# Kernel optimization log

Measured on AMD Instinct MI355X. Metric: run time of the kernel, lower is better.

Reference implementation:

```python
import jax, jax.numpy as jnp
import numpy as np

B, C, H, W_ = 16, 512, 32, 32
NH = 8
DK = C // NH  # 64


def setup_inputs() -> dict:
    key = jax.random.key(0)
    ks = jax.random.split(key, 7)
    s = 1.0 / np.sqrt(C).astype(np.float32)
    x = jax.random.normal(ks[0], (B, C, H, W_), jnp.float32)
    # 1x1 convs == per-pixel channel matmuls; weight shape (out_c, in_c)
    w_q = jax.random.normal(ks[1], (C, C), jnp.float32) * s
    w_k = jax.random.normal(ks[2], (C, C), jnp.float32) * s
    w_v = jax.random.normal(ks[3], (C, C), jnp.float32) * s
    w_o = jax.random.normal(ks[4], (C, C), jnp.float32) * s
    b_o = jnp.zeros((C,), jnp.float32)
    ps = DK ** -0.5
    rel_h = jax.random.normal(ks[5], (2 * H - 1, DK), jnp.float32) * ps
    rel_w = jax.random.normal(ks[6], (2 * W_ - 1, DK), jnp.float32) * ps
    return dict(x=x, w_q=w_q, w_k=w_k, w_v=w_v, w_o=w_o, b_o=b_o,
                rel_h=rel_h, rel_w=rel_w)


def _rel_pos_bias(q, rel_h, rel_w):
    # q: (B, NH, H*W, DK). Content-aware 2D relative position bias:
    # bias[x,y,i,j] = q[x,y]·rel_w[j-y+W-1] + q[x,y]·rel_h[i-x+H-1]
    q4 = q.reshape(B, NH, H, W_, DK)
    idx_w = jnp.arange(W_)[None, :] - jnp.arange(W_)[:, None] + (W_ - 1)  # (Wq,Wk)
    idx_h = jnp.arange(H)[None, :] - jnp.arange(H)[:, None] + (H - 1)     # (Hq,Hk)
    lw = jnp.einsum('bnxyd,rd->bnxyr', q4, rel_w)                # (B,NH,H,W,2W-1)
    aw = jnp.take_along_axis(lw, idx_w[None, None, None], axis=-1)  # (B,NH,H,Wq,Wk)
    lh = jnp.einsum('bnxyd,rd->bnxyr', q4, rel_h)                # (B,NH,H,W,2H-1)
    ah = jnp.take_along_axis(lh.swapaxes(2, 3), idx_h[None, None, None], axis=-1)
    ah = ah.swapaxes(2, 3)                                       # (B,NH,Hq,Wq,Hk)
    bias = ah[..., :, None] + aw[..., None, :]                   # (B,NH,H,W,Hk,Wk)
    return bias.reshape(B, NH, H * W_, H * W_)


def reference(x, w_q, w_k, w_v, w_o, b_o, rel_h, rel_w):
    def proj(w):
        y = jnp.einsum('oc,bchw->bohw', w, x)
        # rearrange 'b (dk h) hi wi -> b h (hi wi) dk' (d_k outer, head inner)
        return y.reshape(B, DK, NH, H * W_).transpose(0, 2, 3, 1)

    q = proj(w_q)  # (B,NH,N,DK), N = H*W
    k = proj(w_k)
    v = proj(w_v)

    energy = jnp.einsum('bnqd,bnkd->bnqk', q, k)
    bias = _rel_pos_bias(q, rel_h, rel_w)
    scores = jax.nn.softmax((energy + bias) / np.sqrt(DK).astype(np.float32), axis=-1)
    out = jnp.einsum('bnqk,bnkd->bnqd', scores, v)
    # rearrange 'b h (hi wi) d -> b (h d) hi wi' (head outer, d_k inner)
    out = out.transpose(0, 1, 3, 2).reshape(B, C, H, W_)
    out = jnp.einsum('oc,bchw->bohw', w_o, out) + b_o[None, :, None, None]
    return out
```

## Files before the change

kernel.cpp:

```cpp
#include <hip/hip_runtime.h>

typedef __attribute__((ext_vector_type(8))) short s8v;
typedef __attribute__((ext_vector_type(4))) float f4v;
typedef __attribute__((ext_vector_type(4))) unsigned short u4v;
typedef __attribute__((ext_vector_type(2))) unsigned int u2v;
typedef __attribute__((ext_vector_type(4))) float fl4;

#define MFMA __builtin_amdgcn_mfma_f32_16x16x32_bf16
#define LOG2E 1.44269504088896340736f
#define QSCALE (0.125f * LOG2E)

__device__ __forceinline__ unsigned short f2bf(float f) {
  return (unsigned short)((__float_as_uint(f) + 0x8000u) >> 16);
}
__device__ __forceinline__ unsigned int pack_bf(float a, float b) {
  return __builtin_amdgcn_perm(__float_as_uint(b) + 0x8000u,
                               __float_as_uint(a) + 0x8000u, 0x07060302u);
}
__device__ __forceinline__ float bf2f(unsigned short u) {
  return __uint_as_float(((unsigned int)u) << 16);
}

__device__ __forceinline__ void gload16(const void* g, void* l) {
  __builtin_amdgcn_global_load_lds(
      (const __attribute__((address_space(1))) unsigned int*)g,
      (__attribute__((address_space(3))) unsigned int*)l,
      16, 0, 0);
}

__device__ __forceinline__ void stage64(unsigned short* lds,
                                        const unsigned short* src,
                                        int src_ld, int tid) {
  const int w = tid >> 6, l = tid & 63;
#pragma unroll
  for (int c = 0; c < 2; ++c) {
    int idx = (c * 4 + w) * 64 + l;
    int row = idx >> 3, cl = idx & 7;
    gload16(src + row * src_ld + ((cl ^ (row & 7)) << 3),
            lds + (c * 4 + w) * 512);
  }
}
__device__ __forceinline__ void stage128(unsigned short* lds,
                                         const unsigned short* src,
                                         int src_ld, int tid) {
  const int w = tid >> 6, l = tid & 63;
#pragma unroll
  for (int c = 0; c < 4; ++c) {
    int id = c * 256 + w * 64 + l;
    int row = id >> 3, cl = id & 7;
    gload16(src + row * src_ld + ((cl ^ (row & 7)) << 3),
            lds + (c * 256 + w * 64) * 8);
  }
}
__device__ __forceinline__ s8v frag64(const unsigned short* lds, int row, int chunk) {
  return *(const s8v*)(lds + row * 64 + ((chunk ^ (row & 7)) << 3));
}

__global__ void cvt_all(const float* __restrict__ wq, const float* __restrict__ wk,
                        const float* __restrict__ wv, const float* __restrict__ wo,
                        const float* __restrict__ relh, const float* __restrict__ relw,
                        unsigned short* __restrict__ Wqkv, unsigned short* __restrict__ Wob,
                        unsigned short* __restrict__ Rel) {
  const int bid = blockIdx.x, tid = threadIdx.x;
  if (bid < 768) {
    int i = bid * 256 + tid;
    int orow = i >> 7, c4 = (i & 127) * 4;
    int p = orow >> 9, oc = orow & 511;
    int h = oc >> 6, d = oc & 63;
    const float* w = (p == 0) ? wq : (p == 1) ? wk : wv;
    fl4 v = *(const fl4*)(w + (d * 8 + h) * 512 + c4);
    u4v o;
    o[0] = f2bf(v[0]); o[1] = f2bf(v[1]); o[2] = f2bf(v[2]); o[3] = f2bf(v[3]);
    *(u4v*)(Wqkv + orow * 512 + c4) = o;
  } else if (bid < 1024) {
    int i = (bid - 768) * 256 + tid;
    fl4 v = ((const fl4*)wo)[i];
    u4v o;
    o[0] = f2bf(v[0]); o[1] = f2bf(v[1]); o[2] = f2bf(v[2]); o[3] = f2bf(v[3]);
    ((u4v*)Wob)[i] = o;
  } else {
    int i = (bid - 1024) * 256 + tid;
    int t = i >> 12, r = (i >> 6) & 63, d = i & 63;
    const float* s = t ? relw : relh;
    Rel[i] = (r < 63) ? f2bf(s[r * 64 + d]) : (unsigned short)0;
  }
}

__global__ void xpose(const float* __restrict__ x, unsigned short* __restrict__ Xt) {
  __shared__ float tls[32][33];
  const int c0 = blockIdx.x * 32, n0 = blockIdx.y * 32, b = blockIdx.z;
  const int tid = threadIdx.x;
  const int rr = tid >> 3, cc4 = (tid & 7) * 4;
  fl4 v = *(const fl4*)(x + (b * 512 + c0 + rr) * 1024 + n0 + cc4);
#pragma unroll
  for (int i = 0; i < 4; ++i) tls[rr][cc4 + i] = v[i];
  __syncthreads();
  u4v o;
#pragma unroll
  for (int i = 0; i < 4; ++i) o[i] = f2bf(tls[cc4 + i][rr]);
  *(u4v*)(Xt + (b * 1024 + n0 + rr) * 512 + c0 + cc4) = o;
}

__global__ __launch_bounds__(256, 2)
void qkv_gemm(const unsigned short* __restrict__ W,
              const unsigned short* __restrict__ Xt,
              unsigned short* __restrict__ qb,
              unsigned short* __restrict__ kb,
              unsigned short* __restrict__ vtb) {
  __shared__ __align__(16) unsigned short Al[8192];
  __shared__ __align__(16) unsigned short Bl[8192];
  const int tid = threadIdx.x, w = tid >> 6, l = tid & 63;
  const int l15 = l & 15, lg = l >> 4;
  const int wr = w >> 1, wc = w & 1;
  const int m0 = blockIdx.x * 128, n0 = blockIdx.y * 128, b = blockIdx.z;
  f4v acc[4][4] = {};
  const unsigned short* As = W + m0 * 512;
  const unsigned short* Bs = Xt + (b * 1024 + n0) * 512;
  for (int k0 = 0; k0 < 512; k0 += 64) {
    stage128(Al, As + k0, 512, tid);
    stage128(Bl, Bs + k0, 512, tid);
    __syncthreads();
#pragma unroll
    for (int kk = 0; kk < 2; ++kk) {
      s8v a[4], bb[4];
#pragma unroll
      for (int i = 0; i < 4; ++i) a[i] = frag64(Al + wr * 4096, i * 16 + l15, kk * 4 + lg);
#pragma unroll
      for (int j = 0; j < 4; ++j) bb[j] = frag64(Bl + wc * 4096, j * 16 + l15, kk * 4 + lg);
#pragma unroll
      for (int i = 0; i < 4; ++i)
#pragma unroll
        for (int j = 0; j < 4; ++j)
          acc[i][j] = MFMA(a[i], bb[j], acc[i][j], 0, 0, 0);
    }
    __syncthreads();
  }
  const int p = m0 >> 9;
  const float sc = (p == 0) ? QSCALE : 1.0f;
#pragma unroll
  for (int i = 0; i < 4; ++i) {
    int o = m0 + wr * 64 + i * 16 + lg * 4;
    int oc = o & 511, hh = oc >> 6, dd = oc & 63;
#pragma unroll
    for (int j = 0; j < 4; ++j) {
      int n = n0 + wc * 64 + j * 16 + l15;
      if (p < 2) {
        u2v pk;
        pk[0] = pack_bf(acc[i][j][0] * sc, acc[i][j][1] * sc);
        pk[1] = pack_bf(acc[i][j][2] * sc, acc[i][j][3] * sc);
        unsigned short* dst = (p == 0 ? qb : kb) + (((b * 8 + hh) * 1024 + n) * 64 + dd);
        *(u2v*)dst = pk;
      } else {
#pragma unroll
        for (int r = 0; r < 4; ++r)
          vtb[((b * 8 + hh) * 64 + dd + r) * 1024 + n] = f2bf(acc[i][j][r]);
      }
    }
  }
}

__global__ __launch_bounds__(256, 4)
void attn_kernel(const unsigned short* __restrict__ qbuf,
                 const unsigned short* __restrict__ kbuf,
                 const unsigned short* __restrict__ vtbuf,
                 const unsigned short* __restrict__ relb,
                 unsigned short* __restrict__ AO) {
  __shared__ __align__(16) unsigned short SH[17152];
  unsigned short* Kl  = SH;
  unsigned short* Vl  = SH + 4096;
  unsigned short* lhb = SH + 8192;
  unsigned short* PwB = SH + 12544;

  const int tid = threadIdx.x, w = tid >> 6, l = tid & 63;
  const int l15 = l & 15, lg = l >> 4;
  const int q0 = blockIdx.x * 64;
  const int bh = blockIdx.z * 8 + blockIdx.y;
  const unsigned short* qh = qbuf + bh * 65536;
  const unsigned short* kh = kbuf + bh * 65536;
  const unsigned short* vh = vtbuf + bh * 65536;
  const int qloc = w * 16 + l15;
  const int qrow = q0 + qloc;
  const int x = qrow >> 5, y = qrow & 31;

  s8v bq[2];
#pragma unroll
  for (int kk = 0; kk < 2; ++kk)
    bq[kk] = *(const s8v*)(qh + qrow * 64 + kk * 32 + lg * 8);

  unsigned short* lwt = SH;
#pragma unroll
  for (int t = 0; t < 2; ++t) {
    unsigned short* dst = t ? lwt : lhb;
#pragma unroll
    for (int ct = 0; ct < 4; ++ct) {
      f4v c = {0.f, 0.f, 0.f, 0.f};
#pragma unroll
      for (int kk = 0; kk < 2; ++kk) {
        s8v a = *(const s8v*)(relb + t * 4096 + (ct * 16 + l15) * 64 + kk * 32 + lg * 8);
        c = MFMA(a, bq[kk], c, 0, 0, 0);
      }
      u2v pk;
      pk[0] = pack_bf(c[0], c[1]);
      pk[1] = pack_bf(c[2], c[3]);
      *(u2v*)(dst + qloc * 68 + ct * 16 + lg * 4) = pk;
    }
  }
  float lwreg[2][4];
#pragma unroll
  for (int c1 = 0; c1 < 2; ++c1)
#pragma unroll
    for (int r = 0; r < 4; ++r)
      lwreg[c1][r] = bf2f(lwt[qloc * 68 + (c1 * 16 + lg * 4 + r) - y + 31]);
  __syncthreads();

  float lsum = 0.f;
  f4v ao[4] = {};
  unsigned short* pw = PwB + w * 1152;

  for (int n0 = 0; n0 < 1024; n0 += 64) {
    stage64(Kl, kh + n0 * 64, 64, tid);
    stage64(Vl, vh + n0, 1024, tid);
    __syncthreads();

    int ib = qloc * 68 + (n0 >> 5) - x + 31;
    float lh0 = bf2f(lhb[ib]);
    float lh1 = bf2f(lhb[ib + 1]);

#pragma unroll
    for (int ct = 0; ct < 4; ++ct) {
      float lh = (ct & 2) ? lh1 : lh0;
      f4v c;
#pragma unroll
      for (int r = 0; r < 4; ++r) c[r] = lh + lwreg[ct & 1][r];
#pragma unroll
      for (int kk = 0; kk < 2; ++kk)
        c = MFMA(frag64(Kl, ct * 16 + l15, kk * 4 + lg), bq[kk], c, 0, 0, 0);
      f4v e;
#pragma unroll
      for (int r = 0; r < 4; ++r) e[r] = __builtin_amdgcn_exp2f(c[r]);
      lsum += (e[0] + e[1]) + (e[2] + e[3]);
      u2v pk;
      pk[0] = pack_bf(e[0], e[1]);
      pk[1] = pack_bf(e[2], e[3]);
      *(u2v*)(pw + l15 * 72 + ct * 16 + lg * 4) = pk;
    }

    s8v ap[2];
#pragma unroll
    for (int kk = 0; kk < 2; ++kk)
      ap[kk] = *(const s8v*)(pw + l15 * 72 + kk * 32 + lg * 8);
#pragma unroll
    for (int dt = 0; dt < 4; ++dt)
#pragma unroll
      for (int kk = 0; kk < 2; ++kk)
        ao[dt] = MFMA(frag64(Vl, dt * 16 + l15, kk * 4 + lg), ap[kk], ao[dt], 0, 0, 0);
    __syncthreads();
  }

  lsum += __shfl_xor(lsum, 16);
  lsum += __shfl_xor(lsum, 32);

  float inv = 1.0f / lsum;
#pragma unroll
  for (int dt = 0; dt < 4; ++dt) {
    u2v pk;
    pk[0] = pack_bf(ao[dt][0] * inv, ao[dt][1] * inv);
    pk[1] = pack_bf(ao[dt][2] * inv, ao[dt][3] * inv);
    *(u2v*)(AO + (bh * 1024 + qrow) * 64 + dt * 16 + lg * 4) = pk;
  }
}

__global__ __launch_bounds__(256, 2)
void out_gemm(const unsigned short* __restrict__ Wo,
              const unsigned short* __restrict__ AO,
              const float* __restrict__ bo,
              float* __restrict__ out) {
  __shared__ __align__(16) unsigned short Al[8192];
  __shared__ __align__(16) unsigned short Bl[8192];
  const int tid = threadIdx.x, w = tid >> 6, l = tid & 63;
  const int l15 = l & 15, lg = l >> 4;
  const int wr = w >> 1, wc = w & 1;
  const int m0 = blockIdx.x * 128, n0 = blockIdx.y * 128, b = blockIdx.z;
  f4v acc[4][4] = {};
  for (int k0 = 0; k0 < 512; k0 += 64) {
    stage128(Al, Wo + m0 * 512 + k0, 512, tid);
    stage128(Bl, AO + ((b * 8 + (k0 >> 6)) * 1024 + n0) * 64, 64, tid);
    __syncthreads();
#pragma unroll
    for (int kk = 0; kk < 2; ++kk) {
      s8v a[4], bb[4];
#pragma unroll
      for (int i = 0; i < 4; ++i) a[i] = frag64(Al + wr * 4096, i * 16 + l15, kk * 4 + lg);
#pragma unroll
      for (int j = 0; j < 4; ++j) bb[j] = frag64(Bl + wc * 4096, j * 16 + l15, kk * 4 + lg);
#pragma unroll
      for (int i = 0; i < 4; ++i)
#pragma unroll
        for (int j = 0; j < 4; ++j)
          acc[i][j] = MFMA(a[i], bb[j], acc[i][j], 0, 0, 0);
    }
    __syncthreads();
  }
#pragma unroll
  for (int i = 0; i < 4; ++i) {
    int ob = m0 + wr * 64 + i * 16 + lg * 4;
    float b0 = bo[ob], b1 = bo[ob + 1], b2 = bo[ob + 2], b3 = bo[ob + 3];
#pragma unroll
    for (int j = 0; j < 4; ++j) {
      int n = n0 + wc * 64 + j * 16 + l15;
      float* op = out + (b * 512 + ob) * 1024 + n;
      op[0]    = acc[i][j][0] + b0;
      op[1024] = acc[i][j][1] + b1;
      op[2048] = acc[i][j][2] + b2;
      op[3072] = acc[i][j][3] + b3;
    }
  }
}


extern "C" void kernel_launch(void* const* d_in, const int* in_sizes, int n_in,
                              void* d_out, int out_size, void* d_ws, size_t ws_size,
                              hipStream_t stream) {
  const float* x    = (const float*)d_in[0];
  const float* wq   = (const float*)d_in[1];
  const float* wk   = (const float*)d_in[2];
  const float* wv   = (const float*)d_in[3];
  const float* wo   = (const float*)d_in[4];
  const float* bo   = (const float*)d_in[5];
  const float* relh = (const float*)d_in[6];
  const float* relw = (const float*)d_in[7];
  char* ws = (char*)d_ws;
  unsigned short* Xt   = (unsigned short*)(ws + 0);
  unsigned short* AO   = (unsigned short*)(ws + 0);
  unsigned short* Wqkv = (unsigned short*)(ws + 16777216);
  unsigned short* Wob  = (unsigned short*)(ws + 18350080);
  unsigned short* Rel  = (unsigned short*)(ws + 18874368);
  unsigned short* Qb   = (unsigned short*)(ws + 18890752);
  unsigned short* Kb   = (unsigned short*)(ws + 35667968);
  unsigned short* Vt   = (unsigned short*)(ws + 52445184);
  float* out = (float*)d_out;

  cvt_all<<<1056, 256, 0, stream>>>(wq, wk, wv, wo, relh, relw, Wqkv, Wob, Rel);
  xpose<<<dim3(16, 32, 16), 256, 0, stream>>>(x, Xt);
  qkv_gemm<<<dim3(12, 8, 16), 256, 0, stream>>>(Wqkv, Xt, Qb, Kb, Vt);
  attn_kernel<<<dim3(16, 8, 16), 256, 0, stream>>>(Qb, Kb, Vt, Rel, AO);
  out_gemm<<<dim3(4, 8, 16), 256, 0, stream>>>(Wob, AO, bo, out);
}
```

Before: 230.8 us.

## Double-buffer K/V tiles in attention and remap block IDs for XCD locality

The attention kernel now keeps two K/V LDS buffers and prefetches the next tile while computing the current one, which halves the barrier count per tile pair and overlaps global loads with MFMA and exp work. The rel-pos projections are reordered so the lw values are read into registers before the lh table overwrites the same LDS region, which drops one sync. All three GEMM/attention grids become 1D with a block-ID remap (bid&7) so that blocks sharing the same data land on the same XCD for L2 reuse. LDS use per attention block grows to about 50KB, which may reduce occupancy below the declared 4 blocks per CU.

```diff
diff --git a/kernel.cpp b/kernel.cpp
--- a/kernel.cpp
+++ b/kernel.cpp
@@ -112,7 +112,11 @@
   const int tid = threadIdx.x, w = tid >> 6, l = tid & 63;
   const int l15 = l & 15, lg = l >> 4;
   const int wr = w >> 1, wc = w & 1;
-  const int m0 = blockIdx.x * 128, n0 = blockIdx.y * 128, b = blockIdx.z;
+  const int bid = blockIdx.x;
+  const int cls = bid & 7, idx = bid >> 3;
+  const int n0 = cls * 128;
+  const int m0 = (idx % 12) * 128;
+  const int b  = idx / 12;
   f4v acc[4][4] = {};
   const unsigned short* As = W + m0 * 512;
   const unsigned short* Bs = Xt + (b * 1024 + n0) * 512;
@@ -165,16 +169,20 @@
                  const unsigned short* __restrict__ vtbuf,
                  const unsigned short* __restrict__ relb,
                  unsigned short* __restrict__ AO) {
-  __shared__ __align__(16) unsigned short SH[17152];
-  unsigned short* Kl  = SH;
-  unsigned short* Vl  = SH + 4096;
-  unsigned short* lhb = SH + 8192;
-  unsigned short* PwB = SH + 12544;
+  __shared__ __align__(16) unsigned short SH[25344];
+  unsigned short* K0  = SH;
+  unsigned short* V0  = SH + 4096;
+  unsigned short* K1  = SH + 8192;
+  unsigned short* V1  = SH + 12288;
+  unsigned short* lhb = SH + 16384;
+  unsigned short* PwB = SH + 20736;
 
   const int tid = threadIdx.x, w = tid >> 6, l = tid & 63;
   const int l15 = l & 15, lg = l >> 4;
-  const int q0 = blockIdx.x * 64;
-  const int bh = blockIdx.z * 8 + blockIdx.y;
+  const int bid = blockIdx.x;
+  const int cls = bid & 7, idx = bid >> 3;
+  const int q0 = (idx & 15) * 64;
+  const int bh = cls + 8 * (idx >> 4);
   const unsigned short* qh = qbuf + bh * 65536;
   const unsigned short* kh = kbuf + bh * 65536;
   const unsigned short* vh = vtbuf + bh * 65536;
@@ -182,50 +190,55 @@
   const int qrow = q0 + qloc;
   const int x = qrow >> 5, y = qrow & 31;
 
+  stage64(K0, kh, 64, tid);
+  stage64(V0, vh, 1024, tid);
+
   s8v bq[2];
 #pragma unroll
   for (int kk = 0; kk < 2; ++kk)
     bq[kk] = *(const s8v*)(qh + qrow * 64 + kk * 32 + lg * 8);
 
-  unsigned short* lwt = SH;
-#pragma unroll
-  for (int t = 0; t < 2; ++t) {
-    unsigned short* dst = t ? lwt : lhb;
-#pragma unroll
-    for (int ct = 0; ct < 4; ++ct) {
-      f4v c = {0.f, 0.f, 0.f, 0.f};
-#pragma unroll
-      for (int kk = 0; kk < 2; ++kk) {
-        s8v a = *(const s8v*)(relb + t * 4096 + (ct * 16 + l15) * 64 + kk * 32 + lg * 8);
-        c = MFMA(a, bq[kk], c, 0, 0, 0);
-      }
-      u2v pk;
-      pk[0] = pack_bf(c[0], c[1]);
-      pk[1] = pack_bf(c[2], c[3]);
-      *(u2v*)(dst + qloc * 68 + ct * 16 + lg * 4) = pk;
-    }
+#pragma unroll
+  for (int ct = 0; ct < 4; ++ct) {
+    f4v c = {0.f, 0.f, 0.f, 0.f};
+#pragma unroll
+    for (int kk = 0; kk < 2; ++kk) {
+      s8v a = *(const s8v*)(relb + 4096 + (ct * 16 + l15) * 64 + kk * 32 + lg * 8);
+      c = MFMA(a, bq[kk], c, 0, 0, 0);
+    }
+    u2v pk;
+    pk[0] = pack_bf(c[0], c[1]);
+    pk[1] = pack_bf(c[2], c[3]);
+    *(u2v*)(lhb + qloc * 68 + ct * 16 + lg * 4) = pk;
   }
   float lwreg[2][4];
 #pragma unroll
   for (int c1 = 0; c1 < 2; ++c1)
 #pragma unroll
     for (int r = 0; r < 4; ++r)
-      lwreg[c1][r] = bf2f(lwt[qloc * 68 + (c1 * 16 + lg * 4 + r) - y + 31]);
-  __syncthreads();
+      lwreg[c1][r] = bf2f(lhb[qloc * 68 + (c1 * 16 + lg * 4 + r) - y + 31]);
+#pragma unroll
+  for (int ct = 0; ct < 4; ++ct) {
+    f4v c = {0.f, 0.f, 0.f, 0.f};
+#pragma unroll
+    for (int kk = 0; kk < 2; ++kk) {
+      s8v a = *(const s8v*)(relb + (ct * 16 + l15) * 64 + kk * 32 + lg * 8);
+      c = MFMA(a, bq[kk], c, 0, 0, 0);
+    }
+    u2v pk;
+    pk[0] = pack_bf(c[0], c[1]);
+    pk[1] = pack_bf(c[2], c[3]);
+    *(u2v*)(lhb + qloc * 68 + ct * 16 + lg * 4) = pk;
+  }
 
   float lsum = 0.f;
   f4v ao[4] = {};
   unsigned short* pw = PwB + w * 1152;
 
-  for (int n0 = 0; n0 < 1024; n0 += 64) {
-    stage64(Kl, kh + n0 * 64, 64, tid);
-    stage64(Vl, vh + n0, 1024, tid);
-    __syncthreads();
-
+  auto tile = [&](const unsigned short* Kc, const unsigned short* Vc, int n0) {
     int ib = qloc * 68 + (n0 >> 5) - x + 31;
     float lh0 = bf2f(lhb[ib]);
     float lh1 = bf2f(lhb[ib + 1]);
-
 #pragma unroll
     for (int ct = 0; ct < 4; ++ct) {
       float lh = (ct & 2) ? lh1 : lh0;
@@ -234,7 +247,7 @@
       for (int r = 0; r < 4; ++r) c[r] = lh + lwreg[ct & 1][r];
 #pragma unroll
       for (int kk = 0; kk < 2; ++kk)
-        c = MFMA(frag64(Kl, ct * 16 + l15, kk * 4 + lg), bq[kk], c, 0, 0, 0);
+        c = MFMA(frag64(Kc, ct * 16 + l15, kk * 4 + lg), bq[kk], c, 0, 0, 0);
       f4v e;
 #pragma unroll
       for (int r = 0; r < 4; ++r) e[r] = __builtin_amdgcn_exp2f(c[r]);
@@ -244,7 +257,6 @@
       pk[1] = pack_bf(e[2], e[3]);
       *(u2v*)(pw + l15 * 72 + ct * 16 + lg * 4) = pk;
     }
-
     s8v ap[2];
 #pragma unroll
     for (int kk = 0; kk < 2; ++kk)
@@ -253,13 +265,25 @@
     for (int dt = 0; dt < 4; ++dt)
 #pragma unroll
       for (int kk = 0; kk < 2; ++kk)
-        ao[dt] = MFMA(frag64(Vl, dt * 16 + l15, kk * 4 + lg), ap[kk], ao[dt], 0, 0, 0);
+        ao[dt] = MFMA(frag64(Vc, dt * 16 + l15, kk * 4 + lg), ap[kk], ao[dt], 0, 0, 0);
+  };
+
+  __syncthreads();
+  for (int t = 0; t < 16; t += 2) {
+    stage64(K1, kh + (t + 1) * 4096, 64, tid);
+    stage64(V1, vh + (t + 1) * 64, 1024, tid);
+    tile(K0, V0, t * 64);
+    __syncthreads();
+    if (t < 14) {
+      stage64(K0, kh + (t + 2) * 4096, 64, tid);
+      stage64(V0, vh + (t + 2) * 64, 1024, tid);
+    }
+    tile(K1, V1, (t + 1) * 64);
     __syncthreads();
   }
 
   lsum += __shfl_xor(lsum, 16);
   lsum += __shfl_xor(lsum, 32);
-
   float inv = 1.0f / lsum;
 #pragma unroll
   for (int dt = 0; dt < 4; ++dt) {
@@ -280,7 +304,11 @@
   const int tid = threadIdx.x, w = tid >> 6, l = tid & 63;
   const int l15 = l & 15, lg = l >> 4;
   const int wr = w >> 1, wc = w & 1;
-  const int m0 = blockIdx.x * 128, n0 = blockIdx.y * 128, b = blockIdx.z;
+  const int bid = blockIdx.x;
+  const int cls = bid & 7, idx = bid >> 3;
+  const int n0 = cls * 128;
+  const int m0 = (idx & 3) * 128;
+  const int b  = idx >> 2;
   f4v acc[4][4] = {};
   for (int k0 = 0; k0 < 512; k0 += 64) {
     stage128(Al, Wo + m0 * 512 + k0, 512, tid);
@@ -342,7 +370,7 @@
 
   cvt_all<<<1056, 256, 0, stream>>>(wq, wk, wv, wo, relh, relw, Wqkv, Wob, Rel);
   xpose<<<dim3(16, 32, 16), 256, 0, stream>>>(x, Xt);
-  qkv_gemm<<<dim3(12, 8, 16), 256, 0, stream>>>(Wqkv, Xt, Qb, Kb, Vt);
-  attn_kernel<<<dim3(16, 8, 16), 256, 0, stream>>>(Qb, Kb, Vt, Rel, AO);
-  out_gemm<<<dim3(4, 8, 16), 256, 0, stream>>>(Wob, AO, bo, out);
-}
+  qkv_gemm<<<1536, 256, 0, stream>>>(Wqkv, Xt, Qb, Kb, Vt);
+  attn_kernel<<<2048, 256, 0, stream>>>(Qb, Kb, Vt, Rel, AO);
+  out_gemm<<<512, 256, 0, stream>>>(Wob, AO, bo, out);
+}
```

After: 230.9 us. No clear change (+0.1%).
